# Kernel tuning notes

Measured on AMD Instinct MI355X. Metric: run time of the kernel, lower is better.

The kernel has to match this reference:

```python
import jax, jax.numpy as jnp
import numpy as np

N = 50000      # nodes
E = 800000     # edges (before self loops)
D_IN = 256     # input feature dim
H = 64         # hidden dim
HEADS = 4
NEG_SLOPE = 0.2  # PyG GATConv default


def setup_inputs() -> dict:
    key = jax.random.key(0)
    ks = jax.random.split(key, 24)

    def w(k, shape, fan_in):
        return jax.random.normal(k, shape, jnp.float32) / np.sqrt(fan_in)

    inp = {
        "x": jax.random.normal(ks[0], (N, D_IN), jnp.float32),
        "edge_index": jax.random.randint(ks[1], (2, E), 0, N, jnp.int64),
        # GCN layers
        "W0": w(ks[2], (D_IN, H), D_IN), "b0": jnp.zeros((H,), jnp.float32),
        "W1": w(ks[3], (H, H), H),       "b1": jnp.zeros((H,), jnp.float32),
        "W2": w(ks[4], (H, H), H),       "b2": jnp.zeros((H,), jnp.float32),
        # GAT
        "Wg": w(ks[5], (H, HEADS * H), H),
        "att_src": w(ks[6], (HEADS, H), H),
        "att_dst": w(ks[7], (HEADS, H), H),
        "bg": jnp.zeros((H,), jnp.float32),
        # classifier MLP: H -> H//2 -> 2
        "Wc1": w(ks[8], (H, H // 2), H),   "bc1": jnp.zeros((H // 2,), jnp.float32),
        "Wc2": w(ks[9], (H // 2, 2), H // 2), "bc2": jnp.zeros((2,), jnp.float32),
        # reconstructor MLP: H -> H -> D_IN
        "Wr1": w(ks[10], (H, H), H),       "br1": jnp.zeros((H,), jnp.float32),
        "Wr2": w(ks[11], (H, D_IN), H),    "br2": jnp.zeros((D_IN,), jnp.float32),
    }
    return inp


def reference(x, edge_index, W0, b0, W1, b1, W2, b2,
              Wg, att_src, att_dst, bg,
              Wc1, bc1, Wc2, bc2, Wr1, br1, Wr2, br2):
    # add self loops (PyG default for both GCNConv and GATConv)
    loops = jnp.arange(N, dtype=edge_index.dtype)
    src = jnp.concatenate([edge_index[0], loops])  # [E+N]
    dst = jnp.concatenate([edge_index[1], loops])

    # symmetric GCN normalization: deg^-1/2[src] * deg^-1/2[dst]
    deg = jax.ops.segment_sum(jnp.ones_like(src, jnp.float32), dst, num_segments=N)
    dinv = jnp.where(deg > 0, jax.lax.rsqrt(deg), 0.0)
    norm = dinv[src] * dinv[dst]  # [E+N]

    def gcn(h, W, b):
        msg = (h @ W)[src] * norm[:, None]          # gather + scale
        return jax.ops.segment_sum(msg, dst, num_segments=N) + b

    # stacked GCN with residuals (dropout inactive in eval)
    h = jax.nn.relu(gcn(x, W0, b0))                 # [N, H]
    h = h + jax.nn.relu(gcn(h, W1, b1))
    h = h + jax.nn.relu(gcn(h, W2, b2))

    # GAT layer, 4 heads, concat=False -> mean over heads
    xg = (h @ Wg).reshape(N, HEADS, H)              # [N, heads, H]
    a_s = jnp.einsum('nhf,hf->nh', xg, att_src)     # [N, heads]
    a_d = jnp.einsum('nhf,hf->nh', xg, att_dst)
    e = jax.nn.leaky_relu(a_s[src] + a_d[dst], NEG_SLOPE)  # [E+N, heads]
    m = jax.ops.segment_max(e, dst, num_segments=N)        # segment softmax
    ex = jnp.exp(e - m[dst])
    s = jax.ops.segment_sum(ex, dst, num_segments=N)
    alpha = ex / s[dst]                                     # [E+N, heads]
    hg = jax.ops.segment_sum(xg[src] * alpha[:, :, None], dst, num_segments=N)
    hg = hg.mean(axis=1) + bg                                # [N, H]

    # global mean pool (batch is None)
    h_global = hg.mean(axis=0, keepdims=True)                # [1, H]
    cls = jax.nn.relu(h_global @ Wc1 + bc1) @ Wc2 + bc2      # [1, 2]
    rec = jax.nn.relu(hg @ Wr1 + br1) @ Wr2 + br2            # [N, D_IN]
    return cls, rec, hg
```

## Files before the change

### kernel.cpp

```cpp
#include <hip/hip_runtime.h>

#define DIN 256
#define HD 64
#define NHEAD 4

static inline int cdiv(long a, long b) { return (int)((a + b - 1) / b); }

typedef __attribute__((ext_vector_type(8))) short bf16x8;
typedef __attribute__((ext_vector_type(4))) float f32x4;

__global__ __launch_bounds__(256) void k_filli(int* __restrict__ p, int v, int n) {
  int i = blockIdx.x * 256 + threadIdx.x;
  if (i < n) p[i] = v;
}

__global__ __launch_bounds__(256) void k_count(const int* __restrict__ dst,
                                               int* __restrict__ cnt, int E) {
  int i = blockIdx.x * 256 + threadIdx.x;
  if (i < E) atomicAdd(&cnt[dst[i]], 1);
}

__global__ __launch_bounds__(256) void k_bsum(const int* __restrict__ cnt,
                                              int* __restrict__ bsum, int n) {
  __shared__ int sd[256];
  int i = blockIdx.x * 256 + threadIdx.x;
  sd[threadIdx.x] = (i < n) ? cnt[i] : 0;
  __syncthreads();
  for (int o = 128; o > 0; o >>= 1) {
    if (threadIdx.x < o) sd[threadIdx.x] += sd[threadIdx.x + o];
    __syncthreads();
  }
  if (threadIdx.x == 0) bsum[blockIdx.x] = sd[0];
}

__global__ __launch_bounds__(256) void k_bscan(const int* __restrict__ bsum,
                                               int* __restrict__ boff, int B) {
  __shared__ int sd[256];
  int t = threadIdx.x;
  int v = (t < B) ? bsum[t] : 0;
  sd[t] = v;
  __syncthreads();
  for (int o = 1; o < 256; o <<= 1) {
    int x = (t >= o) ? sd[t - o] : 0;
    __syncthreads();
    sd[t] += x;
    __syncthreads();
  }
  if (t < B) boff[t] = sd[t] - v;
}

__global__ __launch_bounds__(256) void k_rowptr(const int* __restrict__ cnt,
                                                const int* __restrict__ boff,
                                                int* __restrict__ row_ptr,
                                                int* __restrict__ cursor,
                                                float* __restrict__ dinv,
                                                float* __restrict__ gsum, int n, int total) {
  __shared__ int sd[256];
  int t = threadIdx.x;
  int i = blockIdx.x * 256 + t;
  int v = (i < n) ? cnt[i] : 0;
  sd[t] = v;
  __syncthreads();
  for (int o = 1; o < 256; o <<= 1) {
    int x = (t >= o) ? sd[t - o] : 0;
    __syncthreads();
    sd[t] += x;
    __syncthreads();
  }
  if (i < n) {
    int rp = boff[blockIdx.x] + sd[t] - v;
    row_ptr[i] = rp;
    cursor[i] = rp;
    dinv[i] = rsqrtf((float)v);
  }
  if (i == n - 1) row_ptr[n] = total;
  if (blockIdx.x == 0 && t < 64) gsum[t] = 0.f;
}

__global__ __launch_bounds__(256) void k_csrfill(const int* __restrict__ src,
                                                 const int* __restrict__ dst,
                                                 int* __restrict__ cursor,
                                                 int* __restrict__ csr_src, int E, int n) {
  int e = blockIdx.x * 256 + threadIdx.x;
  if (e < E) {
    int pos = atomicAdd(&cursor[dst[e]], 1);
    csr_src[pos] = src[e];
  } else if (e < E + n) {
    int i = e - E;
    int pos = atomicAdd(&cursor[i], 1);
    csr_src[pos] = i;
  }
}

__device__ __forceinline__ unsigned short f2bf(float f) {
  unsigned u = __float_as_uint(f);
  u += 0x7FFFu + ((u >> 16) & 1u);
  return (unsigned short)(u >> 16);
}
__device__ __forceinline__ float bflo(unsigned u) { return __uint_as_float(u << 16); }
__device__ __forceinline__ float bfhi(unsigned u) { return __uint_as_float(u & 0xFFFF0000u); }

template <int KIN, int KOUT, int ATT, int EPI>
__global__ __launch_bounds__(256, 4) void k_gmfma(const float* __restrict__ A,
                                                  const float* __restrict__ W,
                                                  unsigned short* __restrict__ c16, int n,
                                                  const float* __restrict__ attS,
                                                  const float* __restrict__ attD,
                                                  float* __restrict__ a_s,
                                                  float* __restrict__ a_d,
                                                  const float* __restrict__ bias,
                                                  float* __restrict__ Cf) {
  __shared__ unsigned short As[64][64];
  __shared__ unsigned short Wt[64][64];
  const int tid = threadIdx.x;
  const int m0 = blockIdx.x * 64;
  const int n0 = blockIdx.y * 64;
  const int lane = tid & 63;
  const int wid = tid >> 6;
  const int wm = wid * 16;
  const int fr = lane & 15;
  const int fg = lane >> 4;
  f32x4 acc[4] = {{0.f, 0.f, 0.f, 0.f},
                  {0.f, 0.f, 0.f, 0.f},
                  {0.f, 0.f, 0.f, 0.f},
                  {0.f, 0.f, 0.f, 0.f}};

  for (int k0 = 0; k0 < KIN; k0 += 64) {
    {
      int row = tid >> 3;
      int g = tid & 7;
#pragma unroll
      for (int q = 0; q < 2; ++q, row += 32) {
        int gr = m0 + row;
        gr = gr < n ? gr : n - 1;
        const float* ap = A + (size_t)gr * KIN + k0 + g * 8;
        float4 f0 = *(const float4*)ap;
        float4 f1 = *(const float4*)(ap + 4);
        uint4 pk;
        pk.x = (unsigned)f2bf(f0.x) | ((unsigned)f2bf(f0.y) << 16);
        pk.y = (unsigned)f2bf(f0.z) | ((unsigned)f2bf(f0.w) << 16);
        pk.z = (unsigned)f2bf(f1.x) | ((unsigned)f2bf(f1.y) << 16);
        pk.w = (unsigned)f2bf(f1.z) | ((unsigned)f2bf(f1.w) << 16);
        *(uint4*)&As[row][(g ^ (row & 7)) * 8] = pk;
      }
    }
    {
      int col = tid & 63;
      int kb = (tid >> 6) * 16;
      unsigned pk[8];
#pragma unroll
      for (int i = 0; i < 8; ++i) {
        float lo = W[(size_t)(k0 + kb + 2 * i) * KOUT + n0 + col];
        float hi = W[(size_t)(k0 + kb + 2 * i + 1) * KOUT + n0 + col];
        pk[i] = (unsigned)f2bf(lo) | ((unsigned)f2bf(hi) << 16);
      }
      int g0 = kb >> 3;
      uint4 w0; w0.x = pk[0]; w0.y = pk[1]; w0.z = pk[2]; w0.w = pk[3];
      uint4 w1; w1.x = pk[4]; w1.y = pk[5]; w1.z = pk[6]; w1.w = pk[7];
      *(uint4*)&Wt[col][((g0) ^ (col & 7)) * 8] = w0;
      *(uint4*)&Wt[col][((g0 + 1) ^ (col & 7)) * 8] = w1;
    }
    __syncthreads();
#pragma unroll
    for (int ks = 0; ks < 2; ++ks) {
      int ga = ks * 4 + fg;
      bf16x8 af = *(const bf16x8*)&As[wm + fr][(ga ^ (fr & 7)) * 8];
#pragma unroll
      for (int nt = 0; nt < 4; ++nt) {
        bf16x8 bfr = *(const bf16x8*)&Wt[nt * 16 + fr][(ga ^ (fr & 7)) * 8];
        acc[nt] = __builtin_amdgcn_mfma_f32_16x16x32_bf16(af, bfr, acc[nt], 0, 0, 0);
      }
    }
    __syncthreads();
  }

  if (EPI == 0) {
#pragma unroll
    for (int nt = 0; nt < 4; ++nt) {
#pragma unroll
      for (int r = 0; r < 4; ++r) {
        int row = m0 + wm + fg * 4 + r;
        if (row < n) c16[(size_t)row * KOUT + n0 + nt * 16 + fr] = f2bf(acc[nt][r]);
      }
    }
  } else {
    float bv[4];
#pragma unroll
    for (int nt = 0; nt < 4; ++nt) bv[nt] = bias[n0 + nt * 16 + fr];
#pragma unroll
    for (int nt = 0; nt < 4; ++nt) {
#pragma unroll
      for (int r = 0; r < 4; ++r) {
        int row = m0 + wm + fg * 4 + r;
        float v = acc[nt][r] + bv[nt];
        if (EPI == 1) v = v > 0.f ? v : 0.f;
        if (row < n) Cf[(size_t)row * KOUT + n0 + nt * 16 + fr] = v;
      }
    }
  }
  if (ATT) {
    float attsv[4], attdv[4];
#pragma unroll
    for (int nt = 0; nt < 4; ++nt) {
      attsv[nt] = attS[n0 + nt * 16 + fr];
      attdv[nt] = attD[n0 + nt * 16 + fr];
    }
#pragma unroll
    for (int r = 0; r < 4; ++r) {
      float ps = acc[0][r] * attsv[0] + acc[1][r] * attsv[1] +
                 acc[2][r] * attsv[2] + acc[3][r] * attsv[3];
      float pd = acc[0][r] * attdv[0] + acc[1][r] * attdv[1] +
                 acc[2][r] * attdv[2] + acc[3][r] * attdv[3];
#pragma unroll
      for (int o = 1; o < 16; o <<= 1) {
        ps += __shfl_xor(ps, o);
        pd += __shfl_xor(pd, o);
      }
      int row = m0 + wm + fg * 4 + r;
      if (fr == 0 && row < n) {
        a_s[row * NHEAD + blockIdx.y] = ps;
        a_d[row * NHEAD + blockIdx.y] = pd;
      }
    }
  }
}

__global__ __launch_bounds__(256) void k_agg16(const unsigned short* __restrict__ P16,
                                               const int* __restrict__ csr_src,
                                               const int* __restrict__ row_ptr,
                                               const float* __restrict__ dinv,
                                               const float* __restrict__ bias,
                                               const float* __restrict__ resid,
                                               float* __restrict__ out, int n) {
  int node = (blockIdx.x * 256 + threadIdx.x) >> 6;
  int lane = threadIdx.x & 63;
  if (node >= n) return;
  int beg = row_ptr[node], end = row_ptr[node + 1];
  int es = lane >> 3;
  int fo = (lane & 7) * 8;
  float a[8] = {};
  for (int i = beg + es; i < end; i += 8) {
    int s = csr_src[i];
    float d = dinv[s];
    uint4 v = *(const uint4*)(P16 + (size_t)s * HD + fo);
    a[0] = fmaf(bflo(v.x), d, a[0]); a[1] = fmaf(bfhi(v.x), d, a[1]);
    a[2] = fmaf(bflo(v.y), d, a[2]); a[3] = fmaf(bfhi(v.y), d, a[3]);
    a[4] = fmaf(bflo(v.z), d, a[4]); a[5] = fmaf(bfhi(v.z), d, a[5]);
    a[6] = fmaf(bflo(v.w), d, a[6]); a[7] = fmaf(bfhi(v.w), d, a[7]);
  }
#pragma unroll
  for (int o = 8; o < 64; o <<= 1) {
#pragma unroll
    for (int k = 0; k < 8; ++k) a[k] += __shfl_xor(a[k], o);
  }
  if (lane < 8) {
    float dn = dinv[node];
    float4 b0 = *(const float4*)(bias + fo);
    float4 b1 = *(const float4*)(bias + fo + 4);
    float o0[8];
    o0[0] = a[0] * dn + b0.x; o0[1] = a[1] * dn + b0.y;
    o0[2] = a[2] * dn + b0.z; o0[3] = a[3] * dn + b0.w;
    o0[4] = a[4] * dn + b1.x; o0[5] = a[5] * dn + b1.y;
    o0[6] = a[6] * dn + b1.z; o0[7] = a[7] * dn + b1.w;
#pragma unroll
    for (int k = 0; k < 8; ++k) o0[k] = o0[k] > 0.f ? o0[k] : 0.f;
    if (resid) {
      float4 r0 = *(const float4*)(resid + (size_t)node * HD + fo);
      float4 r1 = *(const float4*)(resid + (size_t)node * HD + fo + 4);
      o0[0] += r0.x; o0[1] += r0.y; o0[2] += r0.z; o0[3] += r0.w;
      o0[4] += r1.x; o0[5] += r1.y; o0[6] += r1.z; o0[7] += r1.w;
    }
    float4 w0; w0.x = o0[0]; w0.y = o0[1]; w0.z = o0[2]; w0.w = o0[3];
    float4 w1; w1.x = o0[4]; w1.y = o0[5]; w1.z = o0[6]; w1.w = o0[7];
    *(float4*)(out + (size_t)node * HD + fo) = w0;
    *(float4*)(out + (size_t)node * HD + fo + 4) = w1;
  }
}

__device__ __forceinline__ float leaky(float v) { return v > 0.f ? v : 0.2f * v; }

__global__ __launch_bounds__(256) void k_gat(const unsigned short* __restrict__ xg16,
                                             const float* __restrict__ a_s,
                                             const float* __restrict__ a_d,
                                             const int* __restrict__ csr_src,
                                             const int* __restrict__ row_ptr,
                                             float* __restrict__ galpha,
                                             const float* __restrict__ bg,
                                             float* __restrict__ hg,
                                             float* __restrict__ hga,
                                             int n) {
  __shared__ float4 ew[4][128];
  const int wid = threadIdx.x >> 6;
  const int node = (blockIdx.x * 256 + threadIdx.x) >> 6;
  const int lane = threadIdx.x & 63;
  if (node >= n) return;
  const int beg = row_ptr[node], end = row_ptr[node + 1];
  const bool uselds = (end - beg) <= 128;
  float4 ad = ((const float4*)a_d)[node];

  float m0 = -1e30f, m1 = -1e30f, m2 = -1e30f, m3 = -1e30f;
  float4 e0, e1;
  const int i0 = beg + lane, i1 = beg + lane + 64;
  if (uselds) {
    if (i0 < end) {
      int s = csr_src[i0];
      float4 as = ((const float4*)a_s)[s];
      e0.x = leaky(as.x + ad.x); e0.y = leaky(as.y + ad.y);
      e0.z = leaky(as.z + ad.z); e0.w = leaky(as.w + ad.w);
      m0 = e0.x; m1 = e0.y; m2 = e0.z; m3 = e0.w;
    }
    if (i1 < end) {
      int s = csr_src[i1];
      float4 as = ((const float4*)a_s)[s];
      e1.x = leaky(as.x + ad.x); e1.y = leaky(as.y + ad.y);
      e1.z = leaky(as.z + ad.z); e1.w = leaky(as.w + ad.w);
      m0 = fmaxf(m0, e1.x); m1 = fmaxf(m1, e1.y);
      m2 = fmaxf(m2, e1.z); m3 = fmaxf(m3, e1.w);
    }
  } else {
    for (int i = i0; i < end; i += 64) {
      int s = csr_src[i];
      float4 as = ((const float4*)a_s)[s];
      float4 e;
      e.x = leaky(as.x + ad.x); e.y = leaky(as.y + ad.y);
      e.z = leaky(as.z + ad.z); e.w = leaky(as.w + ad.w);
      ((float4*)galpha)[i] = e;
      m0 = fmaxf(m0, e.x); m1 = fmaxf(m1, e.y);
      m2 = fmaxf(m2, e.z); m3 = fmaxf(m3, e.w);
    }
    __threadfence();
  }
#pragma unroll
  for (int o = 32; o > 0; o >>= 1) {
    m0 = fmaxf(m0, __shfl_xor(m0, o));
    m1 = fmaxf(m1, __shfl_xor(m1, o));
    m2 = fmaxf(m2, __shfl_xor(m2, o));
    m3 = fmaxf(m3, __shfl_xor(m3, o));
  }

  float s0 = 0.f, s1 = 0.f, s2 = 0.f, s3 = 0.f;
  if (uselds) {
    if (i0 < end) {
      float4 ex;
      ex.x = expf(e0.x - m0); ex.y = expf(e0.y - m1);
      ex.z = expf(e0.z - m2); ex.w = expf(e0.w - m3);
      ew[wid][i0 - beg] = ex;
      s0 += ex.x; s1 += ex.y; s2 += ex.z; s3 += ex.w;
    }
    if (i1 < end) {
      float4 ex;
      ex.x = expf(e1.x - m0); ex.y = expf(e1.y - m1);
      ex.z = expf(e1.z - m2); ex.w = expf(e1.w - m3);
      ew[wid][i1 - beg] = ex;
      s0 += ex.x; s1 += ex.y; s2 += ex.z; s3 += ex.w;
    }
  } else {
    for (int i = i0; i < end; i += 64) {
      float4 e = ((const float4*)galpha)[i];
      float4 ex;
      ex.x = expf(e.x - m0); ex.y = expf(e.y - m1);
      ex.z = expf(e.z - m2); ex.w = expf(e.w - m3);
      ((float4*)galpha)[i] = ex;
      s0 += ex.x; s1 += ex.y; s2 += ex.z; s3 += ex.w;
    }
    __threadfence();
  }
#pragma unroll
  for (int o = 32; o > 0; o >>= 1) {
    s0 += __shfl_xor(s0, o);
    s1 += __shfl_xor(s1, o);
    s2 += __shfl_xor(s2, o);
    s3 += __shfl_xor(s3, o);
  }
  float r0 = 0.25f / s0, r1 = 0.25f / s1, r2 = 0.25f / s2, r3 = 0.25f / s3;

  const int hl = lane & 31;
  const int hw = lane >> 5;
  const int head = hl >> 3;
  float a[8] = {}, b[8] = {};

#define GATHER8(ACC, S, AL)                                                     \
  {                                                                             \
    uint4 v = *(const uint4*)(xg16 + (size_t)(S) * 256 + hl * 8);               \
    ACC[0] = fmaf(bflo(v.x), AL, ACC[0]); ACC[1] = fmaf(bfhi(v.x), AL, ACC[1]); \
    ACC[2] = fmaf(bflo(v.y), AL, ACC[2]); ACC[3] = fmaf(bfhi(v.y), AL, ACC[3]); \
    ACC[4] = fmaf(bflo(v.z), AL, ACC[4]); ACC[5] = fmaf(bfhi(v.z), AL, ACC[5]); \
    ACC[6] = fmaf(bflo(v.w), AL, ACC[6]); ACC[7] = fmaf(bfhi(v.w), AL, ACC[7]); \
  }

#define P3_BODY(ALPHA_AT)                                  \
  {                                                        \
    int i = beg + hw;                                      \
    for (; i + 2 < end; i += 4) {                          \
      int sA = csr_src[i], sB = csr_src[i + 2];            \
      float alA = ALPHA_AT(i), alB = ALPHA_AT(i + 2);      \
      GATHER8(a, sA, alA)                                  \
      GATHER8(b, sB, alB)                                  \
    }                                                      \
    for (; i < end; i += 2) {                              \
      int s = csr_src[i];                                  \
      float al = ALPHA_AT(i);                              \
      GATHER8(a, s, al)                                    \
    }                                                      \
  }

  if (uselds) {
    const float* ap = (const float*)&ew[wid][0];
#define AL_LDS(idx) ap[((idx) - beg) * 4 + head]
    P3_BODY(AL_LDS)
#undef AL_LDS
  } else {
#define AL_GBL(idx) galpha[(size_t)(idx) * 4 + head]
    P3_BODY(AL_GBL)
#undef AL_GBL
  }
#undef P3_BODY
#undef GATHER8

  float rh = head == 0 ? r0 : head == 1 ? r1 : head == 2 ? r2 : r3;
  float t[8];
#pragma unroll
  for (int k = 0; k < 8; ++k) {
    t[k] = a[k] + b[k];
    t[k] += __shfl_xor(t[k], 32);
    t[k] *= rh;
    t[k] += __shfl_xor(t[k], 8);
    t[k] += __shfl_xor(t[k], 16);
  }
  if (lane < 8) {
    int f0 = lane * 8;
    float o0[8];
#pragma unroll
    for (int k = 0; k < 8; ++k) o0[k] = t[k] + bg[f0 + k];
    float4 w0; w0.x = o0[0]; w0.y = o0[1]; w0.z = o0[2]; w0.w = o0[3];
    float4 w1; w1.x = o0[4]; w1.y = o0[5]; w1.z = o0[6]; w1.w = o0[7];
    *(float4*)(hga + (size_t)node * HD + f0) = w0;
    *(float4*)(hga + (size_t)node * HD + f0 + 4) = w1;
    float2 p0; p0.x = o0[0]; p0.y = o0[1];
    float2 p1; p1.x = o0[2]; p1.y = o0[3];
    float2 p2; p2.x = o0[4]; p2.y = o0[5];
    float2 p3; p3.x = o0[6]; p3.y = o0[7];
    *(float2*)(hg + (size_t)node * HD + f0) = p0;
    *(float2*)(hg + (size_t)node * HD + f0 + 2) = p1;
    *(float2*)(hg + (size_t)node * HD + f0 + 4) = p2;
    *(float2*)(hg + (size_t)node * HD + f0 + 6) = p3;
  }
}

__global__ __launch_bounds__(256) void k_gsum(const float* __restrict__ hg,
                                              float* __restrict__ gsum, int n) {
  __shared__ float red[256];
  int f = threadIdx.x & 63, g = threadIdx.x >> 6;
  float local = 0.f;
  for (int nd = blockIdx.x * 4 + g; nd < n; nd += gridDim.x * 4)
    local += hg[(size_t)nd * HD + f];
  red[threadIdx.x] = local;
  __syncthreads();
  if (threadIdx.x < 64)
    atomicAdd(&gsum[f], red[f] + red[64 + f] + red[128 + f] + red[192 + f]);
}

__global__ __launch_bounds__(64) void k_cls(const float* __restrict__ gsum,
                                            const float* __restrict__ Wc1,
                                            const float* __restrict__ bc1,
                                            const float* __restrict__ Wc2,
                                            const float* __restrict__ bc2,
                                            float* __restrict__ out, int n) {
  __shared__ float hgl[64];
  __shared__ float t1[32];
  int t = threadIdx.x;
  hgl[t] = gsum[t] / (float)n;
  __syncthreads();
  if (t < 32) {
    float a = bc1[t];
#pragma unroll 16
    for (int f = 0; f < 64; ++f) a = fmaf(hgl[f], Wc1[f * 32 + t], a);
    t1[t] = a > 0.f ? a : 0.f;
  }
  __syncthreads();
  if (t < 2) {
    float a = bc2[t];
#pragma unroll
    for (int j = 0; j < 32; ++j) a = fmaf(t1[j], Wc2[j * 2 + t], a);
    out[t] = a;
  }
}

extern "C" void kernel_launch(void* const* d_in, const int* in_sizes, int n_in,
                              void* d_out, int out_size, void* d_ws, size_t ws_size,
                              hipStream_t stream) {
  const float* x = (const float*)d_in[0];
  const int* ei = (const int*)d_in[1];
  const float* W0 = (const float*)d_in[2];
  const float* b0 = (const float*)d_in[3];
  const float* W1 = (const float*)d_in[4];
  const float* b1 = (const float*)d_in[5];
  const float* W2 = (const float*)d_in[6];
  const float* b2 = (const float*)d_in[7];
  const float* Wg = (const float*)d_in[8];
  const float* att_src = (const float*)d_in[9];
  const float* att_dst = (const float*)d_in[10];
  const float* bg = (const float*)d_in[11];
  const float* Wc1 = (const float*)d_in[12];
  const float* bc1 = (const float*)d_in[13];
  const float* Wc2 = (const float*)d_in[14];
  const float* bc2 = (const float*)d_in[15];
  const float* Wr1 = (const float*)d_in[16];
  const float* br1 = (const float*)d_in[17];
  const float* Wr2 = (const float*)d_in[18];
  const float* br2 = (const float*)d_in[19];

  const int n = in_sizes[0] / DIN;
  const int E = in_sizes[1] / 2;
  const int nE = E + n;
  const int* src = ei;
  const int* dst = ei + E;

  float* ws = (float*)d_ws;
  size_t off = 0;
  auto alloc = [&](size_t nelems) {
    float* p = ws + off;
    off += (nelems + 63) & ~(size_t)63;
    return p;
  };
  int* CNT = (int*)alloc(n);
  int* BSUM = (int*)alloc(256);
  int* BOFF = (int*)alloc(256);
  int* ROWP = (int*)alloc(n + 1);
  int* CURS = (int*)alloc(n);
  int* CSRS = (int*)alloc(nE);
  float* DINV = alloc(n);
  float* P = alloc((size_t)n * 256);
  unsigned short* XG16 = (unsigned short*)alloc((size_t)n * 128);
  unsigned short* P16 = (unsigned short*)alloc((size_t)n * 32);
  float* Hb = alloc((size_t)n * HD);
  float* HG = alloc((size_t)n * HD);
  float* ASD = alloc((size_t)n * NHEAD);
  float* ADD = alloc((size_t)n * NHEAD);
  float* GALPHA = alloc((size_t)nE * NHEAD);
  float* GSUM = alloc(64);
  (void)ws_size;

  float* out = (float*)d_out;
  float* out_cls = out;
  float* out_rec = out + 2;
  float* out_hg = out + 2 + (size_t)n * 256;

  const int TB = 256;
  const int B = cdiv(n, TB);
  const int GM = cdiv(n, 64);

  k_filli<<<cdiv(n, TB), TB, 0, stream>>>(CNT, 1, n);
  k_count<<<cdiv(E, TB), TB, 0, stream>>>(dst, CNT, E);
  k_bsum<<<B, TB, 0, stream>>>(CNT, BSUM, n);
  k_bscan<<<1, TB, 0, stream>>>(BSUM, BOFF, B);
  k_rowptr<<<B, TB, 0, stream>>>(CNT, BOFF, ROWP, CURS, DINV, GSUM, n, nE);
  k_csrfill<<<cdiv(nE, TB), TB, 0, stream>>>(src, dst, CURS, CSRS, E, n);

  k_gmfma<256, 64, 0, 0><<<dim3(GM, 1), TB, 0, stream>>>(
      x, W0, P16, n, nullptr, nullptr, nullptr, nullptr, nullptr, nullptr);
  k_agg16<<<cdiv((long)n * 64, TB), TB, 0, stream>>>(P16, CSRS, ROWP, DINV, b0, nullptr, Hb, n);

  k_gmfma<64, 64, 0, 0><<<dim3(GM, 1), TB, 0, stream>>>(
      Hb, W1, P16, n, nullptr, nullptr, nullptr, nullptr, nullptr, nullptr);
  k_agg16<<<cdiv((long)n * 64, TB), TB, 0, stream>>>(P16, CSRS, ROWP, DINV, b1, Hb, Hb, n);

  k_gmfma<64, 64, 0, 0><<<dim3(GM, 1), TB, 0, stream>>>(
      Hb, W2, P16, n, nullptr, nullptr, nullptr, nullptr, nullptr, nullptr);
  k_agg16<<<cdiv((long)n * 64, TB), TB, 0, stream>>>(P16, CSRS, ROWP, DINV, b2, Hb, Hb, n);

  k_gmfma<64, 256, 1, 0><<<dim3(GM, 4), TB, 0, stream>>>(
      Hb, Wg, XG16, n, att_src, att_dst, ASD, ADD, nullptr, nullptr);
  k_gat<<<cdiv((long)n * 64, TB), TB, 0, stream>>>(XG16, ASD, ADD, CSRS, ROWP, GALPHA, bg,
                                                   out_hg, HG, n);

  k_gsum<<<512, TB, 0, stream>>>(HG, GSUM, n);
  k_cls<<<1, 64, 0, stream>>>(GSUM, Wc1, bc1, Wc2, bc2, out_cls, n);
  k_gmfma<64, 64, 0, 1><<<dim3(GM, 1), TB, 0, stream>>>(
      HG, Wr1, nullptr, n, nullptr, nullptr, nullptr, nullptr, br1, P);
  k_gmfma<64, 256, 0, 2><<<dim3(GM, 4), TB, 0, stream>>>(
      P, Wr2, nullptr, n, nullptr, nullptr, nullptr, nullptr, br2, out_rec);
}
```

Measured before the change: 352.0 us.

## Fuse reconstructor MLP and global pooling into one kernel, trim CSR setup

Replaces the two reconstructor GEMM launches and the separate global-sum kernel with one fused kernel. It keeps the 64-wide hidden tile in shared memory as bf16, loops over four output column groups, and accumulates the global feature sum with shared-memory atomics. It also merges the block-offset scan into the row-pointer kernel and replaces the fill kernel with a memset, folding the self-loop count in as +1. The GAT kernel no longer writes a duplicate copy of hg. This removes the fp32 intermediate P round trip, several launches and redundant writes. In exchange, every block re-converts Wr2 four times and the pooled sum uses more atomics.

```diff
diff --git a/kernel.cpp b/kernel.cpp
--- a/kernel.cpp
+++ b/kernel.cpp
@@ -8,11 +8,6 @@
 
 typedef __attribute__((ext_vector_type(8))) short bf16x8;
 typedef __attribute__((ext_vector_type(4))) float f32x4;
-
-__global__ __launch_bounds__(256) void k_filli(int* __restrict__ p, int v, int n) {
-  int i = blockIdx.x * 256 + threadIdx.x;
-  if (i < n) p[i] = v;
-}
 
 __global__ __launch_bounds__(256) void k_count(const int* __restrict__ dst,
                                                int* __restrict__ cnt, int E) {
@@ -24,7 +19,7 @@
                                               int* __restrict__ bsum, int n) {
   __shared__ int sd[256];
   int i = blockIdx.x * 256 + threadIdx.x;
-  sd[threadIdx.x] = (i < n) ? cnt[i] : 0;
+  sd[threadIdx.x] = (i < n) ? cnt[i] + 1 : 0;
   __syncthreads();
   for (int o = 128; o > 0; o >>= 1) {
     if (threadIdx.x < o) sd[threadIdx.x] += sd[threadIdx.x + o];
@@ -33,11 +28,27 @@
   if (threadIdx.x == 0) bsum[blockIdx.x] = sd[0];
 }
 
-__global__ __launch_bounds__(256) void k_bscan(const int* __restrict__ bsum,
-                                               int* __restrict__ boff, int B) {
+__global__ __launch_bounds__(256) void k_rowptr(const int* __restrict__ cnt,
+                                                const int* __restrict__ bsum,
+                                                int* __restrict__ row_ptr,
+                                                int* __restrict__ cursor,
+                                                float* __restrict__ dinv,
+                                                float* __restrict__ gsum,
+                                                int n, int total, int B) {
+  __shared__ int sb[256];
   __shared__ int sd[256];
   int t = threadIdx.x;
-  int v = (t < B) ? bsum[t] : 0;
+  sb[t] = (t < B) ? bsum[t] : 0;
+  __syncthreads();
+  for (int o = 1; o < 256; o <<= 1) {
+    int x = (t >= o) ? sb[t - o] : 0;
+    __syncthreads();
+    sb[t] += x;
+    __syncthreads();
+  }
+  int boff = (blockIdx.x > 0) ? sb[blockIdx.x - 1] : 0;
+  int i = blockIdx.x * 256 + t;
+  int v = (i < n) ? cnt[i] + 1 : 0;
   sd[t] = v;
   __syncthreads();
   for (int o = 1; o < 256; o <<= 1) {
@@ -46,29 +57,8 @@
     sd[t] += x;
     __syncthreads();
   }
-  if (t < B) boff[t] = sd[t] - v;
-}
-
-__global__ __launch_bounds__(256) void k_rowptr(const int* __restrict__ cnt,
-                                                const int* __restrict__ boff,
-                                                int* __restrict__ row_ptr,
-                                                int* __restrict__ cursor,
-                                                float* __restrict__ dinv,
-                                                float* __restrict__ gsum, int n, int total) {
-  __shared__ int sd[256];
-  int t = threadIdx.x;
-  int i = blockIdx.x * 256 + t;
-  int v = (i < n) ? cnt[i] : 0;
-  sd[t] = v;
-  __syncthreads();
-  for (int o = 1; o < 256; o <<= 1) {
-    int x = (t >= o) ? sd[t - o] : 0;
-    __syncthreads();
-    sd[t] += x;
-    __syncthreads();
-  }
   if (i < n) {
-    int rp = boff[blockIdx.x] + sd[t] - v;
+    int rp = boff + sd[t] - v;
     row_ptr[i] = rp;
     cursor[i] = rp;
     dinv[i] = rsqrtf((float)v);
@@ -100,16 +90,14 @@
 __device__ __forceinline__ float bflo(unsigned u) { return __uint_as_float(u << 16); }
 __device__ __forceinline__ float bfhi(unsigned u) { return __uint_as_float(u & 0xFFFF0000u); }
 
-template <int KIN, int KOUT, int ATT, int EPI>
+template <int KIN, int KOUT, int ATT>
 __global__ __launch_bounds__(256, 4) void k_gmfma(const float* __restrict__ A,
                                                   const float* __restrict__ W,
                                                   unsigned short* __restrict__ c16, int n,
                                                   const float* __restrict__ attS,
                                                   const float* __restrict__ attD,
                                                   float* __restrict__ a_s,
-                                                  float* __restrict__ a_d,
-                                                  const float* __restrict__ bias,
-                                                  float* __restrict__ Cf) {
+                                                  float* __restrict__ a_d) {
   __shared__ unsigned short As[64][64];
   __shared__ unsigned short Wt[64][64];
   const int tid = threadIdx.x;
@@ -174,28 +162,12 @@
     __syncthreads();
   }
 
-  if (EPI == 0) {
-#pragma unroll
-    for (int nt = 0; nt < 4; ++nt) {
-#pragma unroll
-      for (int r = 0; r < 4; ++r) {
-        int row = m0 + wm + fg * 4 + r;
-        if (row < n) c16[(size_t)row * KOUT + n0 + nt * 16 + fr] = f2bf(acc[nt][r]);
-      }
-    }
-  } else {
-    float bv[4];
-#pragma unroll
-    for (int nt = 0; nt < 4; ++nt) bv[nt] = bias[n0 + nt * 16 + fr];
-#pragma unroll
-    for (int nt = 0; nt < 4; ++nt) {
-#pragma unroll
-      for (int r = 0; r < 4; ++r) {
-        int row = m0 + wm + fg * 4 + r;
-        float v = acc[nt][r] + bv[nt];
-        if (EPI == 1) v = v > 0.f ? v : 0.f;
-        if (row < n) Cf[(size_t)row * KOUT + n0 + nt * 16 + fr] = v;
-      }
+#pragma unroll
+  for (int nt = 0; nt < 4; ++nt) {
+#pragma unroll
+    for (int r = 0; r < 4; ++r) {
+      int row = m0 + wm + fg * 4 + r;
+      if (row < n) c16[(size_t)row * KOUT + n0 + nt * 16 + fr] = f2bf(acc[nt][r]);
     }
   }
   if (ATT) {
@@ -220,6 +192,142 @@
       if (fr == 0 && row < n) {
         a_s[row * NHEAD + blockIdx.y] = ps;
         a_d[row * NHEAD + blockIdx.y] = pd;
+      }
+    }
+  }
+}
+
+__global__ __launch_bounds__(256, 4) void k_rec(const float* __restrict__ hg,
+                                                const float* __restrict__ Wr1,
+                                                const float* __restrict__ br1,
+                                                const float* __restrict__ Wr2,
+                                                const float* __restrict__ br2,
+                                                float* __restrict__ gsum,
+                                                float* __restrict__ rec,
+                                                int n) {
+  __shared__ unsigned short As[64][64];
+  __shared__ unsigned short Ws[64][64];
+  __shared__ unsigned short Ts[64][64];
+  __shared__ float gs[64];
+  const int tid = threadIdx.x;
+  const int m0 = blockIdx.x * 64;
+  const int lane = tid & 63;
+  const int wid = tid >> 6;
+  const int wm = wid * 16;
+  const int fr = lane & 15, fg = lane >> 4;
+
+  if (tid < 64) gs[tid] = 0.f;
+  __syncthreads();
+
+  {
+    int row = tid >> 3, g = tid & 7;
+#pragma unroll
+    for (int q = 0; q < 2; ++q, row += 32) {
+      int gr = m0 + row;
+      bool valid = gr < n;
+      int cr = valid ? gr : n - 1;
+      const float* hp = hg + (size_t)cr * HD + g * 8;
+      float2 f0 = *(const float2*)hp;
+      float2 f1 = *(const float2*)(hp + 2);
+      float2 f2 = *(const float2*)(hp + 4);
+      float2 f3 = *(const float2*)(hp + 6);
+      uint4 pk;
+      pk.x = (unsigned)f2bf(f0.x) | ((unsigned)f2bf(f0.y) << 16);
+      pk.y = (unsigned)f2bf(f1.x) | ((unsigned)f2bf(f1.y) << 16);
+      pk.z = (unsigned)f2bf(f2.x) | ((unsigned)f2bf(f2.y) << 16);
+      pk.w = (unsigned)f2bf(f3.x) | ((unsigned)f2bf(f3.y) << 16);
+      *(uint4*)&As[row][(g ^ (row & 7)) * 8] = pk;
+      if (valid) {
+        atomicAdd(&gs[g * 8 + 0], f0.x); atomicAdd(&gs[g * 8 + 1], f0.y);
+        atomicAdd(&gs[g * 8 + 2], f1.x); atomicAdd(&gs[g * 8 + 3], f1.y);
+        atomicAdd(&gs[g * 8 + 4], f2.x); atomicAdd(&gs[g * 8 + 5], f2.y);
+        atomicAdd(&gs[g * 8 + 6], f3.x); atomicAdd(&gs[g * 8 + 7], f3.y);
+      }
+    }
+  }
+  {
+    int col = tid & 63;
+    int kb = (tid >> 6) * 16;
+    unsigned pk[8];
+#pragma unroll
+    for (int i = 0; i < 8; ++i) {
+      float lo = Wr1[(size_t)(kb + 2 * i) * HD + col];
+      float hi = Wr1[(size_t)(kb + 2 * i + 1) * HD + col];
+      pk[i] = (unsigned)f2bf(lo) | ((unsigned)f2bf(hi) << 16);
+    }
+    int g0 = kb >> 3;
+    uint4 w0; w0.x = pk[0]; w0.y = pk[1]; w0.z = pk[2]; w0.w = pk[3];
+    uint4 w1; w1.x = pk[4]; w1.y = pk[5]; w1.z = pk[6]; w1.w = pk[7];
+    *(uint4*)&Ws[col][((g0) ^ (col & 7)) * 8] = w0;
+    *(uint4*)&Ws[col][((g0 + 1) ^ (col & 7)) * 8] = w1;
+  }
+  __syncthreads();
+  if (tid < 64) atomicAdd(&gsum[tid], gs[tid]);
+
+  {
+    f32x4 acc[4] = {{0.f, 0.f, 0.f, 0.f}, {0.f, 0.f, 0.f, 0.f},
+                    {0.f, 0.f, 0.f, 0.f}, {0.f, 0.f, 0.f, 0.f}};
+#pragma unroll
+    for (int ks = 0; ks < 2; ++ks) {
+      int ga = ks * 4 + fg;
+      bf16x8 af = *(const bf16x8*)&As[wm + fr][(ga ^ (fr & 7)) * 8];
+#pragma unroll
+      for (int nt = 0; nt < 4; ++nt) {
+        bf16x8 bfr = *(const bf16x8*)&Ws[nt * 16 + fr][(ga ^ (fr & 7)) * 8];
+        acc[nt] = __builtin_amdgcn_mfma_f32_16x16x32_bf16(af, bfr, acc[nt], 0, 0, 0);
+      }
+    }
+#pragma unroll
+    for (int nt = 0; nt < 4; ++nt) {
+#pragma unroll
+      for (int r = 0; r < 4; ++r) {
+        int row = wm + fg * 4 + r;
+        int col = nt * 16 + fr;
+        float v = acc[nt][r] + br1[col];
+        v = v > 0.f ? v : 0.f;
+        Ts[row][(((col >> 3) ^ (row & 7)) * 8) + (col & 7)] = f2bf(v);
+      }
+    }
+  }
+
+  for (int cg = 0; cg < 4; ++cg) {
+    __syncthreads();
+    {
+      int col = tid & 63;
+      int kb = (tid >> 6) * 16;
+      unsigned pk[8];
+#pragma unroll
+      for (int i = 0; i < 8; ++i) {
+        float lo = Wr2[(size_t)(kb + 2 * i) * 256 + cg * 64 + col];
+        float hi = Wr2[(size_t)(kb + 2 * i + 1) * 256 + cg * 64 + col];
+        pk[i] = (unsigned)f2bf(lo) | ((unsigned)f2bf(hi) << 16);
+      }
+      int g0 = kb >> 3;
+      uint4 w0; w0.x = pk[0]; w0.y = pk[1]; w0.z = pk[2]; w0.w = pk[3];
+      uint4 w1; w1.x = pk[4]; w1.y = pk[5]; w1.z = pk[6]; w1.w = pk[7];
+      *(uint4*)&Ws[col][((g0) ^ (col & 7)) * 8] = w0;
+      *(uint4*)&Ws[col][((g0 + 1) ^ (col & 7)) * 8] = w1;
+    }
+    __syncthreads();
+    f32x4 acc[4] = {{0.f, 0.f, 0.f, 0.f}, {0.f, 0.f, 0.f, 0.f},
+                    {0.f, 0.f, 0.f, 0.f}, {0.f, 0.f, 0.f, 0.f}};
+#pragma unroll
+    for (int ks = 0; ks < 2; ++ks) {
+      int ga = ks * 4 + fg;
+      bf16x8 af = *(const bf16x8*)&Ts[wm + fr][(ga ^ (fr & 7)) * 8];
+#pragma unroll
+      for (int nt = 0; nt < 4; ++nt) {
+        bf16x8 bfr = *(const bf16x8*)&Ws[nt * 16 + fr][(ga ^ (fr & 7)) * 8];
+        acc[nt] = __builtin_amdgcn_mfma_f32_16x16x32_bf16(af, bfr, acc[nt], 0, 0, 0);
+      }
+    }
+#pragma unroll
+    for (int nt = 0; nt < 4; ++nt) {
+#pragma unroll
+      for (int r = 0; r < 4; ++r) {
+        int row = m0 + wm + fg * 4 + r;
+        int col = cg * 64 + nt * 16 + fr;
+        if (row < n) rec[(size_t)row * 256 + col] = acc[nt][r] + br2[col];
       }
     }
   }
@@ -287,7 +395,6 @@
                                              float* __restrict__ galpha,
                                              const float* __restrict__ bg,
                                              float* __restrict__ hg,
-                                             float* __restrict__ hga,
                                              int n) {
   __shared__ float4 ew[4][128];
   const int wid = threadIdx.x >> 6;
@@ -432,10 +539,6 @@
     float o0[8];
 #pragma unroll
     for (int k = 0; k < 8; ++k) o0[k] = t[k] + bg[f0 + k];
-    float4 w0; w0.x = o0[0]; w0.y = o0[1]; w0.z = o0[2]; w0.w = o0[3];
-    float4 w1; w1.x = o0[4]; w1.y = o0[5]; w1.z = o0[6]; w1.w = o0[7];
-    *(float4*)(hga + (size_t)node * HD + f0) = w0;
-    *(float4*)(hga + (size_t)node * HD + f0 + 4) = w1;
     float2 p0; p0.x = o0[0]; p0.y = o0[1];
     float2 p1; p1.x = o0[2]; p1.y = o0[3];
     float2 p2; p2.x = o0[4]; p2.y = o0[5];
@@ -445,19 +548,6 @@
     *(float2*)(hg + (size_t)node * HD + f0 + 4) = p2;
     *(float2*)(hg + (size_t)node * HD + f0 + 6) = p3;
   }
-}
-
-__global__ __launch_bounds__(256) void k_gsum(const float* __restrict__ hg,
-                                              float* __restrict__ gsum, int n) {
-  __shared__ float red[256];
-  int f = threadIdx.x & 63, g = threadIdx.x >> 6;
-  float local = 0.f;
-  for (int nd = blockIdx.x * 4 + g; nd < n; nd += gridDim.x * 4)
-    local += hg[(size_t)nd * HD + f];
-  red[threadIdx.x] = local;
-  __syncthreads();
-  if (threadIdx.x < 64)
-    atomicAdd(&gsum[f], red[f] + red[64 + f] + red[128 + f] + red[192 + f]);
 }
 
 __global__ __launch_bounds__(64) void k_cls(const float* __restrict__ gsum,
@@ -525,16 +615,13 @@
   };
   int* CNT = (int*)alloc(n);
   int* BSUM = (int*)alloc(256);
-  int* BOFF = (int*)alloc(256);
   int* ROWP = (int*)alloc(n + 1);
   int* CURS = (int*)alloc(n);
   int* CSRS = (int*)alloc(nE);
   float* DINV = alloc(n);
-  float* P = alloc((size_t)n * 256);
   unsigned short* XG16 = (unsigned short*)alloc((size_t)n * 128);
   unsigned short* P16 = (unsigned short*)alloc((size_t)n * 32);
   float* Hb = alloc((size_t)n * HD);
-  float* HG = alloc((size_t)n * HD);
   float* ASD = alloc((size_t)n * NHEAD);
   float* ADD = alloc((size_t)n * NHEAD);
   float* GALPHA = alloc((size_t)nE * NHEAD);
@@ -550,34 +637,29 @@
   const int B = cdiv(n, TB);
   const int GM = cdiv(n, 64);
 
-  k_filli<<<cdiv(n, TB), TB, 0, stream>>>(CNT, 1, n);
+  hipMemsetAsync(CNT, 0, (size_t)n * sizeof(int), stream);
   k_count<<<cdiv(E, TB), TB, 0, stream>>>(dst, CNT, E);
   k_bsum<<<B, TB, 0, stream>>>(CNT, BSUM, n);
-  k_bscan<<<1, TB, 0, stream>>>(BSUM, BOFF, B);
-  k_rowptr<<<B, TB, 0, stream>>>(CNT, BOFF, ROWP, CURS, DINV, GSUM, n, nE);
+  k_rowptr<<<B, TB, 0, stream>>>(CNT, BSUM, ROWP, CURS, DINV, GSUM, n, nE, B);
   k_csrfill<<<cdiv(nE, TB), TB, 0, stream>>>(src, dst, CURS, CSRS, E, n);
 
-  k_gmfma<256, 64, 0, 0><<<dim3(GM, 1), TB, 0, stream>>>(
-      x, W0, P16, n, nullptr, nullptr, nullptr, nullptr, nullptr, nullptr);
+  k_gmfma<256, 64, 0><<<dim3(GM, 1), TB, 0, stream>>>(x, W0, P16, n,
+                                                      nullptr, nullptr, nullptr, nullptr);
   k_agg16<<<cdiv((long)n * 64, TB), TB, 0, stream>>>(P16, CSRS, ROWP, DINV, b0, nullptr, Hb, n);
 
-  k_gmfma<64, 64, 0, 0><<<dim3(GM, 1), TB, 0, stream>>>(
-      Hb, W1, P16, n, nullptr, nullptr, nullptr, nullptr, nullptr, nullptr);
+  k_gmfma<64, 64, 0><<<dim3(GM, 1), TB, 0, stream>>>(Hb, W1, P16, n,
+                                                     nullptr, nullptr, nullptr, nullptr);
   k_agg16<<<cdiv((long)n * 64, TB), TB, 0, stream>>>(P16, CSRS, ROWP, DINV, b1, Hb, Hb, n);
 
-  k_gmfma<64, 64, 0, 0><<<dim3(GM, 1), TB, 0, stream>>>(
-      Hb, W2, P16, n, nullptr, nullptr, nullptr, nullptr, nullptr, nullptr);
+  k_gmfma<64, 64, 0><<<dim3(GM, 1), TB, 0, stream>>>(Hb, W2, P16, n,
+                                                     nullptr, nullptr, nullptr, nullptr);
   k_agg16<<<cdiv((long)n * 64, TB), TB, 0, stream>>>(P16, CSRS, ROWP, DINV, b2, Hb, Hb, n);
 
-  k_gmfma<64, 256, 1, 0><<<dim3(GM, 4), TB, 0, stream>>>(
-      Hb, Wg, XG16, n, att_src, att_dst, ASD, ADD, nullptr, nullptr);
+  k_gmfma<64, 256, 1><<<dim3(GM, 4), TB, 0, stream>>>(Hb, Wg, XG16, n,
+                                                      att_src, att_dst, ASD, ADD);
   k_gat<<<cdiv((long)n * 64, TB), TB, 0, stream>>>(XG16, ASD, ADD, CSRS, ROWP, GALPHA, bg,
-                                                   out_hg, HG, n);
-
-  k_gsum<<<512, TB, 0, stream>>>(HG, GSUM, n);
+                                                   out_hg, n);
+
+  k_rec<<<GM, TB, 0, stream>>>(out_hg, Wr1, br1, Wr2, br2, GSUM, out_rec, n);
   k_cls<<<1, 64, 0, stream>>>(GSUM, Wc1, bc1, Wc2, bc2, out_cls, n);
-  k_gmfma<64, 64, 0, 1><<<dim3(GM, 1), TB, 0, stream>>>(
-      HG, Wr1, nullptr, n, nullptr, nullptr, nullptr, nullptr, br1, P);
-  k_gmfma<64, 256, 0, 2><<<dim3(GM, 4), TB, 0, stream>>>(
-      P, Wr2, nullptr, n, nullptr, nullptr, nullptr, nullptr, br2, out_rec);
-}
+}
```

Measured after the change: 342.7 us, median of 2. -2.6%, faster.
